# Optimization experiments

Hardware: AMD Instinct MI355X
Metric: run time of the kernel (lower is better)

Reference implementation:

```python
import jax, jax.numpy as jnp
import numpy as np

HIDDEN = 4096
NUM_EXPERTS = 64
TOPK = 2
N_TOKENS = 16384


def setup_inputs() -> dict:
    key = jax.random.key(0)
    k_x, k_w, k_b = jax.random.split(key, 3)
    x = jax.random.normal(k_x, (N_TOKENS, HIDDEN), dtype=jnp.float32)
    # torch.nn.Linear: weight [out, in], bias [out], uniform(-1/sqrt(in), 1/sqrt(in))
    bound = 1.0 / np.sqrt(HIDDEN)
    W = jax.random.uniform(k_w, (NUM_EXPERTS, HIDDEN), dtype=jnp.float32, minval=-bound, maxval=bound)
    b = jax.random.uniform(k_b, (NUM_EXPERTS,), dtype=jnp.float32, minval=-bound, maxval=bound)
    return {"x": x, "W": W, "b": b}


def reference(x, W, b):
    # logits: [N, E] = x @ W.T + b
    logits = jnp.einsum("nh,eh->ne", x, W) + b
    probs = jax.nn.softmax(logits, axis=1)
    # torch.topk along dim=1 returns (values, indices), sorted descending
    values, indices = jax.lax.top_k(probs, TOPK)
    return values, indices
```

## Files before the change

kernel.cpp:

```cpp
#include <hip/hip_runtime.h>
#include <math.h>

#define HIDDEN   4096
#define NEXP     64
#define NTOK     16384
#define KCHUNKS  8
#define KC       (HIDDEN / KCHUNKS)
#define BK       16
#define ITERS    (KC / BK)
#define BT       64

__global__ __launch_bounds__(64, 2)
void gemm_partial(const float* __restrict__ x, const float* __restrict__ W,
                  float* __restrict__ part) {
    __shared__ float lds[2][2][64 * BK];

    const int lane = threadIdx.x;
    const int t0   = blockIdx.x * BT;
    const int kbase = blockIdx.y * KC;
    const int i = lane & 7;
    const int j = lane >> 3;

    const int srow = lane >> 2;
    const int sevn = 4 * ((lane & 3) ^ ((lane >> 5) & 3));
    const int sodd = 4 * ((lane & 3) ^ ((2 + (lane >> 5)) & 3));

#define STAGE(buf, itn) do {                                                          \
    _Pragma("unroll")                                                                 \
    for (int p = 0; p < 4; ++p) {                                                     \
        const int ko = kbase + (itn) * BK + ((p & 1) ? sodd : sevn);                  \
        __builtin_amdgcn_global_load_lds(                                             \
            (const __attribute__((address_space(1))) uint32_t*)                       \
                (x + (size_t)(t0 + p * 16 + srow) * HIDDEN + ko),                     \
            (__attribute__((address_space(3))) uint32_t*)&lds[buf][0][p * 256],       \
            16, 0, 0);                                                                \
        __builtin_amdgcn_global_load_lds(                                             \
            (const __attribute__((address_space(1))) uint32_t*)                       \
                (W + (size_t)(p * 16 + srow) * HIDDEN + ko),                          \
            (__attribute__((address_space(3))) uint32_t*)&lds[buf][1][p * 256],       \
            16, 0, 0);                                                                \
    }                                                                                 \
} while (0)

    float acc[8][8];
#pragma unroll
    for (int m = 0; m < 8; ++m)
#pragma unroll
        for (int e = 0; e < 8; ++e) acc[m][e] = 0.f;

    STAGE(0, 0);
    __syncthreads();

    for (int it = 0; it < ITERS; ++it) {
        const int cb = it & 1;
        if (it + 1 < ITERS) STAGE(cb ^ 1, it + 1);

#pragma unroll
        for (int g = 0; g < 4; ++g) {
            float4 WV[8];
#pragma unroll
            for (int e = 0; e < 8; ++e)
                WV[e] = *(const float4*)&lds[cb][1][(j * 8 + e) * BK + 4 * (g ^ (j & 3))];
#pragma unroll
            for (int m = 0; m < 8; ++m) {
                const float4 xq = *(const float4*)&lds[cb][0][(i * 8 + m) * BK + 4 * (g ^ (i & 3))];
#pragma unroll
                for (int e = 0; e < 8; ++e) {
                    float a = fmaf(xq.x, WV[e].x, acc[m][e]);
                    a       = fmaf(xq.y, WV[e].y, a);
                    a       = fmaf(xq.z, WV[e].z, a);
                    acc[m][e] = fmaf(xq.w, WV[e].w, a);
                }
            }
        }
        __syncthreads();
    }
#undef STAGE

    float* dst = part + ((size_t)blockIdx.y * NTOK + t0) * NEXP;
#pragma unroll
    for (int m = 0; m < 8; ++m) {
        const int tok = i * 8 + m;
#pragma unroll
        for (int h = 0; h < 2; ++h) {
            float4 o = make_float4(acc[m][h * 4 + 0], acc[m][h * 4 + 1],
                                   acc[m][h * 4 + 2], acc[m][h * 4 + 3]);
            *(float4*)&dst[(size_t)tok * NEXP + j * 8 + h * 4] = o;
        }
    }
}

__global__ __launch_bounds__(256)
void softmax_top2(const float* __restrict__ part, const float* __restrict__ bias,
                  float* __restrict__ out) {
    const int lane = threadIdx.x & 63;
    const int wid  = threadIdx.x >> 6;
    const int t    = blockIdx.x * 4 + wid;

    float l = bias[lane];
#pragma unroll
    for (int c = 0; c < KCHUNKS; ++c)
        l += part[((size_t)c * NTOK + t) * NEXP + lane];

    float m = l;
#pragma unroll
    for (int s = 32; s > 0; s >>= 1)
        m = fmaxf(m, __shfl_xor(m, s, 64));

    float ssum = expf(l - m);
#pragma unroll
    for (int s = 32; s > 0; s >>= 1)
        ssum += __shfl_xor(ssum, s, 64);

    float v1 = l; int i1 = lane;
#pragma unroll
    for (int s = 32; s > 0; s >>= 1) {
        float ov = __shfl_xor(v1, s, 64);
        int   oi = __shfl_xor(i1, s, 64);
        if (ov > v1 || (ov == v1 && oi < i1)) { v1 = ov; i1 = oi; }
    }
    float v2 = (lane == i1) ? -INFINITY : l;
    int   i2 = lane;
#pragma unroll
    for (int s = 32; s > 0; s >>= 1) {
        float ov = __shfl_xor(v2, s, 64);
        int   oi = __shfl_xor(i2, s, 64);
        if (ov > v2 || (ov == v2 && oi < i2)) { v2 = ov; i2 = oi; }
    }

    if (lane == 0) {
        const float inv = 1.0f / ssum;
        out[(size_t)t * 2 + 0] = inv;
        out[(size_t)t * 2 + 1] = expf(v2 - m) * inv;
        out[(size_t)2 * NTOK + t * 2 + 0] = (float)i1;
        out[(size_t)2 * NTOK + t * 2 + 1] = (float)i2;
    }
}

extern "C" void kernel_launch(void* const* d_in, const int* in_sizes, int n_in,
                              void* d_out, int out_size, void* d_ws, size_t ws_size,
                              hipStream_t stream) {
    const float* x  = (const float*)d_in[0];
    const float* W  = (const float*)d_in[1];
    const float* b  = (const float*)d_in[2];
    float* out  = (float*)d_out;
    float* part = (float*)d_ws;

    dim3 g1(NTOK / BT, KCHUNKS);
    gemm_partial<<<g1, 64, 0, stream>>>(x, W, part);
    softmax_top2<<<NTOK / 4, 256, 0, stream>>>(part, b, out);
}
```

Baseline: 411.3 us.

## Split GEMM tile across two waves by expert half, sharing staged loads

The partial GEMM block grows from one wave to two. Each wave computes 32 of the 64 experts for the same 64-token tile, and each wave stages either the x tile or the W tile into LDS. This halves the per-thread accumulator and register footprint so more waves can be resident, and it shares the LDS tile between the two waves. In exchange the per-wave arithmetic intensity drops: each wave reads x from LDS for only 4 experts per lane instead of 8. The lane-to-(i,j) mapping and the swizzle indexing are also recomputed.

```diff
diff --git a/kernel.cpp b/kernel.cpp
--- a/kernel.cpp
+++ b/kernel.cpp
@@ -10,20 +10,23 @@
 #define ITERS    (KC / BK)
 #define BT       64
 
-__global__ __launch_bounds__(64, 2)
+__global__ __launch_bounds__(128, 4)
 void gemm_partial(const float* __restrict__ x, const float* __restrict__ W,
                   float* __restrict__ part) {
     __shared__ float lds[2][2][64 * BK];
 
-    const int lane = threadIdx.x;
+    const int tid  = threadIdx.x;
+    const int lane = tid & 63;
+    const int eh   = tid >> 6;
     const int t0   = blockIdx.x * BT;
     const int kbase = blockIdx.y * KC;
-    const int i = lane & 7;
-    const int j = lane >> 3;
+    const int i = lane >> 3;
+    const int j = lane & 7;
 
     const int srow = lane >> 2;
     const int sevn = 4 * ((lane & 3) ^ ((lane >> 5) & 3));
     const int sodd = 4 * ((lane & 3) ^ ((2 + (lane >> 5)) & 3));
+    const float* sbase = (eh == 0) ? (x + (size_t)t0 * HIDDEN) : W;
 
 #define STAGE(buf, itn) do {                                                          \
     _Pragma("unroll")                                                                 \
@@ -31,22 +34,17 @@
         const int ko = kbase + (itn) * BK + ((p & 1) ? sodd : sevn);                  \
         __builtin_amdgcn_global_load_lds(                                             \
             (const __attribute__((address_space(1))) uint32_t*)                       \
-                (x + (size_t)(t0 + p * 16 + srow) * HIDDEN + ko),                     \
-            (__attribute__((address_space(3))) uint32_t*)&lds[buf][0][p * 256],       \
-            16, 0, 0);                                                                \
-        __builtin_amdgcn_global_load_lds(                                             \
-            (const __attribute__((address_space(1))) uint32_t*)                       \
-                (W + (size_t)(p * 16 + srow) * HIDDEN + ko),                          \
-            (__attribute__((address_space(3))) uint32_t*)&lds[buf][1][p * 256],       \
+                (sbase + (size_t)(p * 16 + srow) * HIDDEN + ko),                      \
+            (__attribute__((address_space(3))) uint32_t*)&lds[buf][eh][p * 256],      \
             16, 0, 0);                                                                \
     }                                                                                 \
 } while (0)
 
-    float acc[8][8];
+    float acc[8][4];
 #pragma unroll
     for (int m = 0; m < 8; ++m)
 #pragma unroll
-        for (int e = 0; e < 8; ++e) acc[m][e] = 0.f;
+        for (int e = 0; e < 4; ++e) acc[m][e] = 0.f;
 
     STAGE(0, 0);
     __syncthreads();
@@ -57,15 +55,18 @@
 
 #pragma unroll
         for (int g = 0; g < 4; ++g) {
-            float4 WV[8];
+            float4 WV[4];
 #pragma unroll
-            for (int e = 0; e < 8; ++e)
-                WV[e] = *(const float4*)&lds[cb][1][(j * 8 + e) * BK + 4 * (g ^ (j & 3))];
+            for (int e = 0; e < 4; ++e) {
+                const int rw = eh * 32 + j * 4 + e;
+                WV[e] = *(const float4*)&lds[cb][1][rw * BK + 4 * (g ^ ((rw >> 3) & 3))];
+            }
 #pragma unroll
             for (int m = 0; m < 8; ++m) {
-                const float4 xq = *(const float4*)&lds[cb][0][(i * 8 + m) * BK + 4 * (g ^ (i & 3))];
+                const int rx = i * 8 + m;
+                const float4 xq = *(const float4*)&lds[cb][0][rx * BK + 4 * (g ^ ((rx >> 3) & 3))];
 #pragma unroll
-                for (int e = 0; e < 8; ++e) {
+                for (int e = 0; e < 4; ++e) {
                     float a = fmaf(xq.x, WV[e].x, acc[m][e]);
                     a       = fmaf(xq.y, WV[e].y, a);
                     a       = fmaf(xq.z, WV[e].z, a);
@@ -77,16 +78,12 @@
     }
 #undef STAGE
 
-    float* dst = part + ((size_t)blockIdx.y * NTOK + t0) * NEXP;
+    float* dst = part + ((size_t)blockIdx.y * NTOK + t0) * NEXP + eh * 32;
 #pragma unroll
     for (int m = 0; m < 8; ++m) {
         const int tok = i * 8 + m;
-#pragma unroll
-        for (int h = 0; h < 2; ++h) {
-            float4 o = make_float4(acc[m][h * 4 + 0], acc[m][h * 4 + 1],
-                                   acc[m][h * 4 + 2], acc[m][h * 4 + 3]);
-            *(float4*)&dst[(size_t)tok * NEXP + j * 8 + h * 4] = o;
-        }
+        *(float4*)&dst[(size_t)tok * NEXP + j * 4] =
+            make_float4(acc[m][0], acc[m][1], acc[m][2], acc[m][3]);
     }
 }
 
@@ -147,6 +144,6 @@
     float* part = (float*)d_ws;
 
     dim3 g1(NTOK / BT, KCHUNKS);
-    gemm_partial<<<g1, 64, 0, stream>>>(x, W, part);
+    gemm_partial<<<g1, 128, 0, stream>>>(x, W, part);
     softmax_top2<<<NTOK / 4, 256, 0, stream>>>(part, b, out);
 }
```

After: 457.8 us. 1.11x slower.
